# Performance work log

Measured on AMD Instinct MI355X. Metric: run time of the kernel, lower is better.

## Reference

```python
import jax, jax.numpy as jnp
import numpy as np

REP_THR = 0.6
BORDER = 10


def setup_inputs() -> dict:
    key = jax.random.key(0)
    repeatability = jax.random.uniform(key, (8, 1, 2048, 2048), dtype=jnp.float32)
    return {"repeatability": repeatability}


def reference(repeatability):
    # 3x3 max pool, stride 1, pad 1 (torch pads with -inf for max pool)
    local_max = jax.lax.reduce_window(
        repeatability,
        -jnp.inf,
        jax.lax.max,
        window_dimensions=(1, 1, 3, 3),
        window_strides=(1, 1, 1, 1),
        padding=[(0, 0), (0, 0), (1, 1), (1, 1)],
    )
    maxima = (repeatability == local_max) & (repeatability >= REP_THR)
    # border mask: zero out a 10-pixel frame
    B, C, H, W = repeatability.shape
    border = jnp.zeros((H, W), dtype=bool).at[BORDER:-BORDER, BORDER:-BORDER].set(True)
    maxima = maxima & border  # broadcast over (B, C)
    # Original returns maxima.nonzero().t()[2:4] (data-dependent shape);
    # for jit-compatibility we return the dense boolean mask as float32 —
    # the (y, x) indices are exactly the nonzero positions of this mask.
    return maxima.astype(jnp.float32)
```

## Files before the change

### kernel.cpp

```cpp
#include <hip/hip_runtime.h>
#include <math.h>

#define IMG_H 2048
#define IMG_W 2048
#define NB    8
#define BORDER 10
#define REP_THR 0.6f
#define ROWS 16

typedef float f32x4 __attribute__((ext_vector_type(4)));

__global__ __launch_bounds__(256) void nms_kernel(const float* __restrict__ in,
                                                  float* __restrict__ out) {
    const int tid = blockIdx.x * blockDim.x + threadIdx.x;
    const int gx  = tid & 511;
    const int gys = (tid >> 9) & 127;
    const int b   = tid >> 16;

    const int x4 = gx << 2;
    const int y0 = gys << 4;

    const size_t img_off = (size_t)b * IMG_H * IMG_W;
    float* obase = out + img_off + (size_t)y0 * IMG_W + x4;

    if (gx == 0 || gx == 511) {
        const f32x4 z = {0.f, 0.f, 0.f, 0.f};
#pragma unroll
        for (int j = 0; j < ROWS; ++j)
            __builtin_nontemporal_store(z, (f32x4*)(obase + (size_t)j * IMG_W));
        return;
    }

    const float* ibase = in + img_off + x4;
    const int rlo = BORDER - 1;
    const int rhi = IMG_H - BORDER;

#define LOADROW(r, v, h) do {                                             \
        int rc_ = (r);                                                    \
        rc_ = rc_ < rlo ? rlo : (rc_ > rhi ? rhi : rc_);                  \
        const float* row_ = ibase + (size_t)rc_ * IMG_W;                  \
        (v) = *(const f32x4*)row_;                                        \
        const float l_ = row_[-1];                                        \
        const float q_ = row_[4];                                         \
        (h)[0] = fmaxf(l_,     fmaxf((v)[0], (v)[1]));                    \
        (h)[1] = fmaxf((v)[0], fmaxf((v)[1], (v)[2]));                    \
        (h)[2] = fmaxf((v)[1], fmaxf((v)[2], (v)[3]));                    \
        (h)[3] = fmaxf((v)[2], fmaxf((v)[3], q_));                        \
    } while (0)

    f32x4 vA, hA, vB, hB;
    LOADROW(y0 - 1, vA, hA);
    LOADROW(y0,     vB, hB);
    (void)vA;

    const bool bx0 = (x4 + 0 >= BORDER) && (x4 + 0 < IMG_W - BORDER);
    const bool bx1 = (x4 + 1 >= BORDER) && (x4 + 1 < IMG_W - BORDER);
    const bool bx2 = (x4 + 2 >= BORDER) && (x4 + 2 < IMG_W - BORDER);
    const bool bx3 = (x4 + 3 >= BORDER) && (x4 + 3 < IMG_W - BORDER);

#pragma unroll
    for (int j = 0; j < ROWS; ++j) {
        const int y = y0 + j;

        f32x4 vC, hC;
        LOADROW(y + 1, vC, hC);

        f32x4 m;
        m[0] = fmaxf(hA[0], fmaxf(hB[0], hC[0]));
        m[1] = fmaxf(hA[1], fmaxf(hB[1], hC[1]));
        m[2] = fmaxf(hA[2], fmaxf(hB[2], hC[2]));
        m[3] = fmaxf(hA[3], fmaxf(hB[3], hC[3]));

        const bool rowok = (y >= BORDER) && (y < IMG_H - BORDER);

        f32x4 r;
        r[0] = (vB[0] == m[0] && vB[0] >= REP_THR && bx0 && rowok) ? 1.f : 0.f;
        r[1] = (vB[1] == m[1] && vB[1] >= REP_THR && bx1 && rowok) ? 1.f : 0.f;
        r[2] = (vB[2] == m[2] && vB[2] >= REP_THR && bx2 && rowok) ? 1.f : 0.f;
        r[3] = (vB[3] == m[3] && vB[3] >= REP_THR && bx3 && rowok) ? 1.f : 0.f;

        __builtin_nontemporal_store(r, (f32x4*)(obase + (size_t)j * IMG_W));

        hA = hB;
        vB = vC;
        hB = hC;
    }
#undef LOADROW
}

extern "C" void kernel_launch(void* const* d_in, const int* in_sizes, int n_in,
                              void* d_out, int out_size, void* d_ws, size_t ws_size,
                              hipStream_t stream) {
    const float* in = (const float*)d_in[0];
    float* out = (float*)d_out;
    const int total_threads = NB * (IMG_H / ROWS) * (IMG_W / 4);
    const int block = 256;
    const int grid = total_threads / block;
    nms_kernel<<<grid, block, 0, stream>>>(in, out);
}
```

Baseline: 235.7 us.

## Halve rows per thread and issue all row loads upfront before compute

Result: faster. 230.1 us (-2.4%).

```diff
diff --git a/kernel.cpp b/kernel.cpp
--- a/kernel.cpp
+++ b/kernel.cpp
@@ -6,7 +6,7 @@
 #define NB    8
 #define BORDER 10
 #define REP_THR 0.6f
-#define ROWS 16
+#define ROWS 8
 
 typedef float f32x4 __attribute__((ext_vector_type(4)));
 
@@ -14,16 +14,16 @@
                                                   float* __restrict__ out) {
     const int tid = blockIdx.x * blockDim.x + threadIdx.x;
     const int gx  = tid & 511;
-    const int gys = (tid >> 9) & 127;
-    const int b   = tid >> 16;
+    const int gys = (tid >> 9) & 255;
+    const int b   = tid >> 17;
 
     const int x4 = gx << 2;
-    const int y0 = gys << 4;
+    const int y0 = gys << 3;
 
     const size_t img_off = (size_t)b * IMG_H * IMG_W;
     float* obase = out + img_off + (size_t)y0 * IMG_W + x4;
 
-    if (gx == 0 || gx == 511) {
+    if (gx == 0 || gx == 511 || y0 + ROWS <= BORDER || y0 >= IMG_H - BORDER) {
         const f32x4 z = {0.f, 0.f, 0.f, 0.f};
 #pragma unroll
         for (int j = 0; j < ROWS; ++j)
@@ -32,26 +32,28 @@
     }
 
     const float* ibase = in + img_off + x4;
-    const int rlo = BORDER - 1;
-    const int rhi = IMG_H - BORDER;
 
-#define LOADROW(r, v, h) do {                                             \
-        int rc_ = (r);                                                    \
-        rc_ = rc_ < rlo ? rlo : (rc_ > rhi ? rhi : rc_);                  \
-        const float* row_ = ibase + (size_t)rc_ * IMG_W;                  \
-        (v) = *(const f32x4*)row_;                                        \
-        const float l_ = row_[-1];                                        \
-        const float q_ = row_[4];                                         \
-        (h)[0] = fmaxf(l_,     fmaxf((v)[0], (v)[1]));                    \
-        (h)[1] = fmaxf((v)[0], fmaxf((v)[1], (v)[2]));                    \
-        (h)[2] = fmaxf((v)[1], fmaxf((v)[2], (v)[3]));                    \
-        (h)[3] = fmaxf((v)[2], fmaxf((v)[3], q_));                        \
-    } while (0)
+    f32x4 v[ROWS + 2];
+    float l[ROWS + 2], q[ROWS + 2];
+#pragma unroll
+    for (int r = 0; r < ROWS + 2; ++r) {
+        int rc = y0 - 1 + r;
+        rc = rc < (BORDER - 1) ? (BORDER - 1)
+           : (rc > (IMG_H - BORDER) ? (IMG_H - BORDER) : rc);
+        const float* row = ibase + (size_t)rc * IMG_W;
+        v[r] = *(const f32x4*)row;
+        l[r] = row[-1];
+        q[r] = row[4];
+    }
 
-    f32x4 vA, hA, vB, hB;
-    LOADROW(y0 - 1, vA, hA);
-    LOADROW(y0,     vB, hB);
-    (void)vA;
+    f32x4 h[ROWS + 2];
+#pragma unroll
+    for (int r = 0; r < ROWS + 2; ++r) {
+        h[r][0] = fmaxf(l[r],    fmaxf(v[r][0], v[r][1]));
+        h[r][1] = fmaxf(v[r][0], fmaxf(v[r][1], v[r][2]));
+        h[r][2] = fmaxf(v[r][1], fmaxf(v[r][2], v[r][3]));
+        h[r][3] = fmaxf(v[r][2], fmaxf(v[r][3], q[r]));
+    }
 
     const bool bx0 = (x4 + 0 >= BORDER) && (x4 + 0 < IMG_W - BORDER);
     const bool bx1 = (x4 + 1 >= BORDER) && (x4 + 1 < IMG_W - BORDER);
@@ -61,31 +63,23 @@
 #pragma unroll
     for (int j = 0; j < ROWS; ++j) {
         const int y = y0 + j;
-
-        f32x4 vC, hC;
-        LOADROW(y + 1, vC, hC);
+        const bool rowok = (y >= BORDER) && (y < IMG_H - BORDER);
 
         f32x4 m;
-        m[0] = fmaxf(hA[0], fmaxf(hB[0], hC[0]));
-        m[1] = fmaxf(hA[1], fmaxf(hB[1], hC[1]));
-        m[2] = fmaxf(hA[2], fmaxf(hB[2], hC[2]));
-        m[3] = fmaxf(hA[3], fmaxf(hB[3], hC[3]));
+        m[0] = fmaxf(h[j][0], fmaxf(h[j + 1][0], h[j + 2][0]));
+        m[1] = fmaxf(h[j][1], fmaxf(h[j + 1][1], h[j + 2][1]));
+        m[2] = fmaxf(h[j][2], fmaxf(h[j + 1][2], h[j + 2][2]));
+        m[3] = fmaxf(h[j][3], fmaxf(h[j + 1][3], h[j + 2][3]));
 
-        const bool rowok = (y >= BORDER) && (y < IMG_H - BORDER);
-
+        const f32x4 c = v[j + 1];
         f32x4 r;
-        r[0] = (vB[0] == m[0] && vB[0] >= REP_THR && bx0 && rowok) ? 1.f : 0.f;
-        r[1] = (vB[1] == m[1] && vB[1] >= REP_THR && bx1 && rowok) ? 1.f : 0.f;
-        r[2] = (vB[2] == m[2] && vB[2] >= REP_THR && bx2 && rowok) ? 1.f : 0.f;
-        r[3] = (vB[3] == m[3] && vB[3] >= REP_THR && bx3 && rowok) ? 1.f : 0.f;
+        r[0] = (c[0] == m[0] && c[0] >= REP_THR && bx0 && rowok) ? 1.f : 0.f;
+        r[1] = (c[1] == m[1] && c[1] >= REP_THR && bx1 && rowok) ? 1.f : 0.f;
+        r[2] = (c[2] == m[2] && c[2] >= REP_THR && bx2 && rowok) ? 1.f : 0.f;
+        r[3] = (c[3] == m[3] && c[3] >= REP_THR && bx3 && rowok) ? 1.f : 0.f;
 
         __builtin_nontemporal_store(r, (f32x4*)(obase + (size_t)j * IMG_W));
-
-        hA = hB;
-        vB = vC;
-        hB = hC;
     }
-#undef LOADROW
 }
 
 extern "C" void kernel_launch(void* const* d_in, const int* in_sizes, int n_in,
```
